# Optimization experiments

Measured on AMD Instinct MI355X. Metric: run time of the kernel, lower is better.

Reference implementation:

```python
import jax, jax.numpy as jnp
import numpy as np

NEG_SLOPE = 0.2  # PyG GATConv default leaky_relu slope


def gat_conv(x, src, dst, W, att_src, att_dst, bias, num_nodes):
    """PyG-style GATConv with concat=False (mean over heads).
    x: [N, Fin], src/dst: [E] (self-loops already appended),
    W: [Fin, H*C], att_src/att_dst: [H, C], bias: [C].
    """
    H, C = att_src.shape
    h = (x @ W).reshape(num_nodes, H, C)               # [N, H, C]
    a_s = jnp.sum(h * att_src[None], axis=-1)          # [N, H]
    a_d = jnp.sum(h * att_dst[None], axis=-1)          # [N, H]
    e = jax.nn.leaky_relu(a_s[src] + a_d[dst], NEG_SLOPE)  # [E, H]
    # softmax over incoming edges per destination node
    e_max = jax.ops.segment_max(e, dst, num_segments=num_nodes)  # [N, H]
    e_exp = jnp.exp(e - e_max[dst])
    denom = jax.ops.segment_sum(e_exp, dst, num_segments=num_nodes)
    alpha = e_exp / (denom[dst] + 1e-16)               # [E, H]
    msg = h[src] * alpha[:, :, None]                   # [E, H, C]
    out = jax.ops.segment_sum(msg, dst, num_segments=num_nodes)  # [N, H, C]
    return out.mean(axis=1) + bias                     # concat=False -> head mean


def setup_inputs() -> dict:
    N, E = 100000, 1600000
    Fin, Hid, Fout, Hds = 128, 64, 32, 2
    key = jax.random.key(0)
    ks = jax.random.split(key, 12)
    glorot = lambda k, shape, fan: (jax.random.normal(k, shape, jnp.float32) / np.sqrt(fan))
    return {
        "x": jax.random.normal(ks[0], (N, Fin), jnp.float32),
        "edge_index": jax.random.randint(ks[1], (2, E), 0, N, jnp.int64 if jax.config.read("jax_enable_x64") else jnp.int32),
        "W1": glorot(ks[2], (Fin, Hds * Hid), Fin),
        "att_src1": glorot(ks[3], (Hds, Hid), Hid),
        "att_dst1": glorot(ks[4], (Hds, Hid), Hid),
        "b1": jnp.zeros((Hid,), jnp.float32),
        "W2": glorot(ks[5], (Hid, Hds * Fout), Hid),
        "att_src2": glorot(ks[6], (Hds, Fout), Fout),
        "att_dst2": glorot(ks[7], (Hds, Fout), Fout),
        "b2": jnp.zeros((Fout,), jnp.float32),
    }


def reference(x, edge_index, W1, att_src1, att_dst1, b1, W2, att_src2, att_dst2, b2):
    N = x.shape[0]
    # PyG GATConv default: add self-loops
    loops = jnp.arange(N, dtype=edge_index.dtype)
    src = jnp.concatenate([edge_index[0], loops])
    dst = jnp.concatenate([edge_index[1], loops])
    # dropout(p=0.6) is identity in eval mode
    h = gat_conv(x, src, dst, W1, att_src1, att_dst1, b1, N)
    h = jax.nn.elu(h)
    out = gat_conv(h, src, dst, W2, att_src2, att_dst2, b2, N)
    return out
```

## Files before the change

kernel.cpp:

```cpp
#include <hip/hip_runtime.h>
#include <hip/hip_bf16.h>
#include <hip/hip_fp16.h>
#include <math.h>


#define BINBITS 9
#define NBUCK 256
#define CHUNK 4096
#define SPANCAP 12288

typedef _Float16 half8 __attribute__((ext_vector_type(8)));
typedef float f32x4 __attribute__((ext_vector_type(4)));


__global__ void init_kernel(int* __restrict__ bcnt) {
    bcnt[threadIdx.x] = 0;
}

__global__ void bucket_hist_kernel(const int* __restrict__ dst, int* __restrict__ bcnt, int E) {
    __shared__ int h[NBUCK];
    int t = threadIdx.x;
    h[t] = 0;
    __syncthreads();
    for (int i = blockIdx.x * blockDim.x + t; i < E; i += gridDim.x * blockDim.x)
        atomicAdd(&h[dst[i] >> BINBITS], 1);
    __syncthreads();
    if (h[t]) atomicAdd(&bcnt[t], h[t]);
}

__global__ void bucket_scan_kernel(const int* __restrict__ bcnt, int* __restrict__ bbase,
                                   int* __restrict__ bfill) {
    __shared__ int sd[NBUCK];
    int t = threadIdx.x;
    int v = bcnt[t];
    sd[t] = v;
    __syncthreads();
    for (int o = 1; o < NBUCK; o <<= 1) {
        int x = (t >= o) ? sd[t - o] : 0;
        __syncthreads();
        sd[t] += x;
        __syncthreads();
    }
    int exc = sd[t] - v;
    bbase[t] = exc;
    bfill[t] = exc;
    if (t == NBUCK - 1) bbase[NBUCK] = sd[t];
}

__launch_bounds__(256)
__global__ void binA_kernel(const int* __restrict__ esrc, const int* __restrict__ edst,
                            int* __restrict__ bfill, unsigned* __restrict__ binned, int E) {
    __shared__ unsigned stage[CHUNK];
    __shared__ int hcnt[NBUCK], hexc[NBUCK], gb[NBUCK], hfill[NBUCK];
    const int tid = threadIdx.x;
    const int c0 = blockIdx.x * CHUNK;
    const int n = min(CHUNK, E - c0);

    hcnt[tid] = 0;
    hfill[tid] = 0;
    __syncthreads();
    for (int i = tid; i < n; i += 256) atomicAdd(&hcnt[edst[c0 + i] >> BINBITS], 1);
    __syncthreads();
    int myc = hcnt[tid];
    hexc[tid] = myc;
    __syncthreads();
    for (int o = 1; o < NBUCK; o <<= 1) {
        int x = (tid >= o) ? hexc[tid - o] : 0;
        __syncthreads();
        hexc[tid] += x;
        __syncthreads();
    }
    hexc[tid] -= myc;
    gb[tid] = myc ? atomicAdd(&bfill[tid], myc) : 0;
    __syncthreads();

    for (int i = tid; i < n; i += 256) {
        int d = edst[c0 + i], s = esrc[c0 + i];
        int b = d >> BINBITS;
        int p = hexc[b] + atomicAdd(&hfill[b], 1);
        stage[p] = ((unsigned)(d & ((1 << BINBITS) - 1)) << 17) | (unsigned)s;
    }
    __syncthreads();

    const int wid = tid >> 6, lane = tid & 63;
    for (int b = wid * 64; b < wid * 64 + 64; ++b) {
        int cnt = hcnt[b], sb = hexc[b], g = gb[b];
        for (int l = lane; l < cnt; l += 64) binned[g + l] = stage[sb + l];
    }
}

__launch_bounds__(256)
__global__ void binB_kernel(const unsigned* __restrict__ binned, const int* __restrict__ bbase,
                            int* __restrict__ rowptr, int* __restrict__ csr, int N) {
    __shared__ int cnt[512];
    __shared__ int chunk[256];
    __shared__ int excl[513];
    __shared__ int stag[SPANCAP];
    const int tid = threadIdx.x;
    const int b = blockIdx.x;
    const int node0 = b << BINBITS;
    if (node0 >= N) return;
    const int nn = min(512, N - node0);

    cnt[tid] = (tid < nn) ? 1 : 0;
    cnt[tid + 256] = (tid + 256 < nn) ? 1 : 0;
    __syncthreads();
    const int e0 = bbase[b], e1 = bbase[b + 1];
    for (int i = e0 + tid; i < e1; i += 256)
        atomicAdd(&cnt[binned[i] >> 17], 1);
    __syncthreads();

    int c0v = cnt[2 * tid], c1v = cnt[2 * tid + 1];
    chunk[tid] = c0v + c1v;
    __syncthreads();
    int v = chunk[tid];
    for (int o = 1; o < 256; o <<= 1) {
        int x = (tid >= o) ? chunk[tid - o] : 0;
        __syncthreads();
        chunk[tid] += x;
        __syncthreads();
    }
    int cpre = chunk[tid] - v;
    excl[2 * tid] = cpre;
    excl[2 * tid + 1] = cpre + c0v;
    if (tid == 255) excl[512] = cpre + c0v + c1v;
    __syncthreads();

    const int rbase = e0 + node0;
    for (int i = tid; i < nn; i += 256) rowptr[node0 + i] = rbase + excl[i];
    if (node0 + nn >= N && tid == 0) rowptr[N] = rbase + excl[512];

    cnt[tid] = 0;
    cnt[tid + 256] = 0;
    __syncthreads();
    const int span = excl[512];

    if (span <= SPANCAP) {
        for (int i = e0 + tid; i < e1; i += 256) {
            unsigned e = binned[i];
            int dloc = e >> 17, src = e & 0x1FFFF;
            int p = excl[dloc] + atomicAdd(&cnt[dloc], 1);
            stag[p] = src;
        }
        for (int i = tid; i < nn; i += 256) {
            int p = excl[i] + atomicAdd(&cnt[i], 1);
            stag[p] = node0 + i;
        }
        __syncthreads();
        for (int i = tid; i < span; i += 256) csr[rbase + i] = stag[i];
    } else {
        for (int i = e0 + tid; i < e1; i += 256) {
            unsigned e = binned[i];
            int dloc = e >> 17, src = e & 0x1FFFF;
            csr[rbase + excl[dloc] + atomicAdd(&cnt[dloc], 1)] = src;
        }
        for (int i = tid; i < nn; i += 256)
            csr[rbase + excl[i] + atomicAdd(&cnt[i], 1)] = node0 + i;
    }
}


__global__ void wcvt_kernel(const float* __restrict__ W, _Float16* __restrict__ Wt,
                            int K, int Fout) {
    int i = blockIdx.x * 256 + threadIdx.x;
    if (i < K * Fout) {
        int n = i / K, k = i % K;
        Wt[i] = (_Float16)W[k * Fout + n];
    }
}


template <int FIN, int FOUT, typename XT>
__launch_bounds__(256)
__global__ void gemm_attn_mfma(const XT* __restrict__ X, const _Float16* __restrict__ Wt,
                               const float* __restrict__ atts, const float* __restrict__ attd,
                               __half* __restrict__ Hh, float* __restrict__ a_s,
                               float* __restrict__ a_d, int N) {
    constexpr int BM = 128;
    constexpr int C = FOUT / 2;
    constexpr int NT = FOUT / 16;
    constexpr int KS = FIN / 32;
    constexpr int HT = C / 16;
    __shared__ _Float16 sA[BM * FIN];
    __shared__ _Float16 sB[FOUT * FIN];

    const int tid = threadIdx.x;
    const int wv = tid >> 6, ln = tid & 63;
    const int lm = ln & 15, quad = ln >> 4;
    const int row0 = blockIdx.x * BM;

    if (sizeof(XT) == 4) {
        for (int idx = tid; idx < BM * FIN / 4; idx += 256) {
            int r = idx / (FIN / 4), c4 = idx % (FIN / 4);
            int gr = row0 + r;
            float4 v = make_float4(0.f, 0.f, 0.f, 0.f);
            if (gr < N) v = *(const float4*)&((const float*)X)[(size_t)gr * FIN + c4 * 4];
            _Float16 h4[4] = {(_Float16)v.x, (_Float16)v.y, (_Float16)v.z, (_Float16)v.w};
            *(float2*)&sA[r * FIN + c4 * 4] = *(float2*)h4;
        }
    } else {
        for (int idx = tid; idx < BM * FIN / 8; idx += 256) {
            int r = idx / (FIN / 8), c8 = idx % (FIN / 8);
            int gr = row0 + r;
            int4 v = make_int4(0, 0, 0, 0);
            if (gr < N) v = *(const int4*)&((const __half*)X)[(size_t)gr * FIN + c8 * 8];
            *(int4*)&sA[r * FIN + c8 * 8] = v;
        }
    }
    for (int idx = tid; idx < FOUT * FIN / 8; idx += 256)
        *(int4*)&sB[idx * 8] = *(const int4*)&Wt[idx * 8];
    __syncthreads();

    f32x4 acc[2][NT];
#pragma unroll
    for (int mt = 0; mt < 2; ++mt)
#pragma unroll
        for (int nt = 0; nt < NT; ++nt) acc[mt][nt] = f32x4{0.f, 0.f, 0.f, 0.f};

    const int r0 = wv * 32 + lm;
#pragma unroll
    for (int ks = 0; ks < KS; ++ks) {
        int k0 = ks * 32 + quad * 8;
        half8 a0 = *(const half8*)&sA[r0 * FIN + k0];
        half8 a1 = *(const half8*)&sA[(r0 + 16) * FIN + k0];
#pragma unroll
        for (int nt = 0; nt < NT; ++nt) {
            half8 b = *(const half8*)&sB[(nt * 16 + lm) * FIN + k0];
            acc[0][nt] = __builtin_amdgcn_mfma_f32_16x16x32_f16(a0, b, acc[0][nt], 0, 0, 0);
            acc[1][nt] = __builtin_amdgcn_mfma_f32_16x16x32_f16(a1, b, acc[1][nt], 0, 0, 0);
        }
    }

    float psum[2][4][2], pdum[2][4][2];
#pragma unroll
    for (int mt = 0; mt < 2; ++mt)
#pragma unroll
        for (int r = 0; r < 4; ++r) {
            psum[mt][r][0] = psum[mt][r][1] = 0.f;
            pdum[mt][r][0] = pdum[mt][r][1] = 0.f;
        }
#pragma unroll
    for (int nt = 0; nt < NT; ++nt) {
        float av = atts[nt * 16 + lm];
        float dv = attd[nt * 16 + lm];
        int hh = nt / HT;
#pragma unroll
        for (int mt = 0; mt < 2; ++mt)
#pragma unroll
            for (int r = 0; r < 4; ++r) {
                psum[mt][r][hh] = fmaf(acc[mt][nt][r], av, psum[mt][r][hh]);
                pdum[mt][r][hh] = fmaf(acc[mt][nt][r], dv, pdum[mt][r][hh]);
            }
    }
#pragma unroll
    for (int o = 1; o < 16; o <<= 1) {
#pragma unroll
        for (int mt = 0; mt < 2; ++mt)
#pragma unroll
            for (int r = 0; r < 4; ++r) {
                psum[mt][r][0] += __shfl_xor(psum[mt][r][0], o);
                psum[mt][r][1] += __shfl_xor(psum[mt][r][1], o);
                pdum[mt][r][0] += __shfl_xor(pdum[mt][r][0], o);
                pdum[mt][r][1] += __shfl_xor(pdum[mt][r][1], o);
            }
    }
    if (lm == 0) {
#pragma unroll
        for (int mt = 0; mt < 2; ++mt)
#pragma unroll
            for (int r = 0; r < 4; ++r) {
                int gr = row0 + wv * 32 + mt * 16 + quad * 4 + r;
                if (gr < N) {
                    *(float2*)&a_s[gr * 2] = make_float2(psum[mt][r][0], psum[mt][r][1]);
                    *(float2*)&a_d[gr * 2] = make_float2(pdum[mt][r][0], pdum[mt][r][1]);
                }
            }
    }

    __syncthreads();
    _Float16* sH = sA;
#pragma unroll
    for (int mt = 0; mt < 2; ++mt)
#pragma unroll
        for (int nt = 0; nt < NT; ++nt)
#pragma unroll
            for (int r = 0; r < 4; ++r)
                sH[(wv * 32 + mt * 16 + quad * 4 + r) * FOUT + nt * 16 + lm] =
                    (_Float16)acc[mt][nt][r];
    __syncthreads();
    for (int idx = tid; idx < BM * FOUT / 8; idx += 256) {
        int r = idx / (FOUT / 8), c8 = idx % (FOUT / 8);
        int gr = row0 + r;
        if (gr < N)
            *(int4*)&Hh[(size_t)gr * FOUT + c8 * 8] = *(const int4*)&sH[r * FOUT + c8 * 8];
    }
}


__device__ __forceinline__ float lrelu02(float x) { return x > 0.f ? x : 0.2f * x; }

__launch_bounds__(256)
__global__ void edge_w_kernel(const float* __restrict__ a_s, const float* __restrict__ a_d,
                              const int* __restrict__ rowptr, const int* __restrict__ csr,
                              float2* __restrict__ w, int N) {
    const int wid = threadIdx.x >> 6, lane = threadIdx.x & 63;
    int n = blockIdx.x * 4 + wid;
    if (n >= N) return;
    int start = rowptr[n], end = rowptr[n + 1];
    float2 adn = ((const float2*)a_d)[n];
    float d0 = 0.f, d1 = 0.f;
    for (int j = start + lane; j < end; j += 64) {
        int s = csr[j];
        float2 asv = ((const float2*)a_s)[s];
        float e0 = __expf(lrelu02(asv.x + adn.x));
        float e1 = __expf(lrelu02(asv.y + adn.y));
        d0 += e0;
        d1 += e1;
        w[j] = make_float2(e0, e1);
    }
#pragma unroll
    for (int o = 32; o > 0; o >>= 1) {
        d0 += __shfl_xor(d0, o);
        d1 += __shfl_xor(d1, o);
    }
    float i0 = 0.5f / d0, i1 = 0.5f / d1;
    for (int j = start + lane; j < end; j += 64) {
        float2 f = w[j];
        w[j] = make_float2(f.x * i0, f.y * i1);
    }
}


template <int C, bool ELU, typename OT>
__launch_bounds__(256)
__global__ void aggregate_kernel(const __half* __restrict__ Hh, const float2* __restrict__ w,
                                 const int* __restrict__ rowptr, const int* __restrict__ csr,
                                 const float* __restrict__ bias, OT* __restrict__ out, int N) {
    __shared__ float2 swH[4][64][2];
    const int wid = threadIdx.x >> 6;
    const int lane = threadIdx.x & 63;
    const int hp = lane >> 5;
    const int sub = lane & 31;
    const int head = sub >> 4;
    const int chq = sub & 15;
    int n = blockIdx.x * 4 + wid;
    if (n >= N) return;
    int start = rowptr[n], end = rowptr[n + 1];

    float acc0 = 0.f, acc1 = 0.f, acc2 = 0.f, acc3 = 0.f;

    for (int cs = start; cs < end; cs += 64) {
        int j = cs + lane;
        float2 wv = make_float2(0.f, 0.f);
        int s = 0;
        if (j < end) {
            s = csr[j];
            wv = w[j];
        }
        float fs = __int_as_float(s);
        swH[wid][lane][0] = make_float2(wv.x, fs);
        swH[wid][lane][1] = make_float2(wv.y, fs);
        int cnt = min(64, end - cs);
        int npair = (cnt + 1) >> 1;
        for (int p0 = 0; p0 < npair; p0 += 4) {
            float2 e[4];
#pragma unroll
            for (int u = 0; u < 4; ++u)
                e[u] = swH[wid][2 * (p0 + u) + hp][head];
            if (C == 64) {
                ushort4 hv[4];
#pragma unroll
                for (int u = 0; u < 4; ++u)
                    hv[u] = ((const ushort4*)Hh)[(size_t)__float_as_int(e[u].y) * 32 + sub];
#pragma unroll
                for (int u = 0; u < 4; ++u) {
                    const __half* hx = (const __half*)&hv[u];
                    acc0 = fmaf(e[u].x, __half2float(hx[0]), acc0);
                    acc1 = fmaf(e[u].x, __half2float(hx[1]), acc1);
                    acc2 = fmaf(e[u].x, __half2float(hx[2]), acc2);
                    acc3 = fmaf(e[u].x, __half2float(hx[3]), acc3);
                }
            } else {
                __half2 hv[4];
#pragma unroll
                for (int u = 0; u < 4; ++u)
                    hv[u] = ((const __half2*)Hh)[(size_t)__float_as_int(e[u].y) * 32 + sub];
#pragma unroll
                for (int u = 0; u < 4; ++u) {
                    float2 v = __half22float2(hv[u]);
                    acc0 = fmaf(e[u].x, v.x, acc0);
                    acc1 = fmaf(e[u].x, v.y, acc1);
                }
            }
        }
    }

    acc0 += __shfl_xor(acc0, 32);
    acc1 += __shfl_xor(acc1, 32);
    if (C == 64) {
        acc2 += __shfl_xor(acc2, 32);
        acc3 += __shfl_xor(acc3, 32);
    }
    acc0 += __shfl_xor(acc0, 16);
    acc1 += __shfl_xor(acc1, 16);
    if (C == 64) {
        acc2 += __shfl_xor(acc2, 16);
        acc3 += __shfl_xor(acc3, 16);
    }

    if (lane < 16) {
        if (C == 64) {
            float4 bv = *(const float4*)(bias + chq * 4);
            float o0 = acc0 + bv.x;
            float o1 = acc1 + bv.y;
            float o2 = acc2 + bv.z;
            float o3 = acc3 + bv.w;
            if (ELU) {
                o0 = o0 > 0.f ? o0 : expm1f(o0);
                o1 = o1 > 0.f ? o1 : expm1f(o1);
                o2 = o2 > 0.f ? o2 : expm1f(o2);
                o3 = o3 > 0.f ? o3 : expm1f(o3);
            }
            if (sizeof(OT) == 2) {
                __half2 p0 = __floats2half2_rn(o0, o1);
                __half2 p1 = __floats2half2_rn(o2, o3);
                ((__half2*)out)[(size_t)n * 32 + chq * 2] = p0;
                ((__half2*)out)[(size_t)n * 32 + chq * 2 + 1] = p1;
            } else {
                *(float4*)((float*)out + (size_t)n * 64 + chq * 4) =
                    make_float4(o0, o1, o2, o3);
            }
        } else {
            float2 bv = *(const float2*)(bias + chq * 2);
            float o0 = acc0 + bv.x;
            float o1 = acc1 + bv.y;
            if (ELU) {
                o0 = o0 > 0.f ? o0 : expm1f(o0);
                o1 = o1 > 0.f ? o1 : expm1f(o1);
            }
            *(float2*)((float*)out + (size_t)n * 32 + chq * 2) = make_float2(o0, o1);
        }
    }
}


extern "C" void kernel_launch(void* const* d_in, const int* in_sizes, int n_in,
                              void* d_out, int out_size, void* d_ws, size_t ws_size,
                              hipStream_t stream) {
    const float* x    = (const float*)d_in[0];
    const int*   eidx = (const int*)d_in[1];
    const float* W1   = (const float*)d_in[2];
    const float* as1w = (const float*)d_in[3];
    const float* ad1w = (const float*)d_in[4];
    const float* b1   = (const float*)d_in[5];
    const float* W2   = (const float*)d_in[6];
    const float* as2w = (const float*)d_in[7];
    const float* ad2w = (const float*)d_in[8];
    const float* b2   = (const float*)d_in[9];
    float* out = (float*)d_out;

    const int N = in_sizes[0] / 128;
    const int E = in_sizes[1] / 2;
    const int NBK = (N + (1 << BINBITS) - 1) >> BINBITS;

    char* base = (char*)d_ws;
    size_t off = 0;
    auto alloc = [&](size_t bytes) {
        size_t cur = off;
        off += (bytes + 255) & ~(size_t)255;
        return (void*)(base + cur);
    };

    int* rowptr   = (int*)alloc((size_t)(N + 1) * 4);
    int* csr      = (int*)alloc((size_t)(E + N) * 4);
    int* bcnt     = (int*)alloc((size_t)NBUCK * 4);
    int* bbase    = (int*)alloc((size_t)(NBUCK + 1) * 4);
    int* bfill    = (int*)alloc((size_t)NBUCK * 4);
    unsigned* binned = (unsigned*)alloc((size_t)E * 4);
    __half* h1    = (__half*)alloc((size_t)N * 128 * 2);
    __half* x2h   = (__half*)alloc((size_t)N * 64 * 2);
    float* a_s    = (float*)alloc((size_t)N * 2 * 4);
    float* a_d    = (float*)alloc((size_t)N * 2 * 4);
    float2* wEdge = (float2*)alloc((size_t)(E + N) * 8);
    _Float16* Wt1 = (_Float16*)alloc((size_t)128 * 128 * 2);
    _Float16* Wt2 = (_Float16*)alloc((size_t)64 * 64 * 2);

    const int* esrc = eidx;
    const int* edst = eidx + E;

    init_kernel<<<1, NBUCK, 0, stream>>>(bcnt);
    bucket_hist_kernel<<<256, 256, 0, stream>>>(edst, bcnt, E);
    bucket_scan_kernel<<<1, NBUCK, 0, stream>>>(bcnt, bbase, bfill);
    binA_kernel<<<(E + CHUNK - 1) / CHUNK, 256, 0, stream>>>(esrc, edst, bfill, binned, E);
    binB_kernel<<<NBK, 256, 0, stream>>>(binned, bbase, rowptr, csr, N);

    wcvt_kernel<<<(128 * 128 + 255) / 256, 256, 0, stream>>>(W1, Wt1, 128, 128);
    wcvt_kernel<<<(64 * 64 + 255) / 256, 256, 0, stream>>>(W2, Wt2, 64, 64);

    gemm_attn_mfma<128, 128, float>
        <<<(N + 127) / 128, 256, 0, stream>>>(x, Wt1, as1w, ad1w, h1, a_s, a_d, N);
    edge_w_kernel<<<(N + 3) / 4, 256, 0, stream>>>(a_s, a_d, rowptr, csr, wEdge, N);
    aggregate_kernel<64, true, __half>
        <<<(N + 3) / 4, 256, 0, stream>>>(h1, wEdge, rowptr, csr, b1, x2h, N);

    gemm_attn_mfma<64, 64, __half>
        <<<(N + 127) / 128, 256, 0, stream>>>(x2h, Wt2, as2w, ad2w, h1, a_s, a_d, N);
    edge_w_kernel<<<(N + 3) / 4, 256, 0, stream>>>(a_s, a_d, rowptr, csr, wEdge, N);
    aggregate_kernel<32, false, float>
        <<<(N + 3) / 4, 256, 0, stream>>>(h1, wEdge, rowptr, csr, b2, out, N);
}
```

Baseline: 374.6 us.

## Widen aggregate gathers to 16-byte loads, add single-pass edge softmax, merge weight conversions

```diff
diff --git a/kernel.cpp b/kernel.cpp
--- a/kernel.cpp
+++ b/kernel.cpp
@@ -160,12 +160,17 @@
 }
 
 
-__global__ void wcvt_kernel(const float* __restrict__ W, _Float16* __restrict__ Wt,
-                            int K, int Fout) {
+__global__ void wcvt_kernel(const float* __restrict__ W1, _Float16* __restrict__ Wt1,
+                            const float* __restrict__ W2, _Float16* __restrict__ Wt2) {
     int i = blockIdx.x * 256 + threadIdx.x;
-    if (i < K * Fout) {
-        int n = i / K, k = i % K;
-        Wt[i] = (_Float16)W[k * Fout + n];
+    if (i < 128 * 128) {
+        int n = i >> 7, k = i & 127;
+        Wt1[i] = (_Float16)W1[k * 128 + n];
+    }
+    int j = i - 128 * 128;
+    if (j >= 0 && j < 64 * 64) {
+        int n = j >> 6, k = j & 63;
+        Wt2[j] = (_Float16)W2[k * 64 + n];
     }
 }
 
@@ -307,26 +312,47 @@
     int n = blockIdx.x * 4 + wid;
     if (n >= N) return;
     int start = rowptr[n], end = rowptr[n + 1];
+    int deg = end - start;
     float2 adn = ((const float2*)a_d)[n];
-    float d0 = 0.f, d1 = 0.f;
-    for (int j = start + lane; j < end; j += 64) {
-        int s = csr[j];
-        float2 asv = ((const float2*)a_s)[s];
-        float e0 = __expf(lrelu02(asv.x + adn.x));
-        float e1 = __expf(lrelu02(asv.y + adn.y));
-        d0 += e0;
-        d1 += e1;
-        w[j] = make_float2(e0, e1);
-    }
-#pragma unroll
-    for (int o = 32; o > 0; o >>= 1) {
-        d0 += __shfl_xor(d0, o);
-        d1 += __shfl_xor(d1, o);
-    }
-    float i0 = 0.5f / d0, i1 = 0.5f / d1;
-    for (int j = start + lane; j < end; j += 64) {
-        float2 f = w[j];
-        w[j] = make_float2(f.x * i0, f.y * i1);
+
+    if (deg <= 64) {
+        float e0 = 0.f, e1 = 0.f;
+        int j = start + lane;
+        if (lane < deg) {
+            int s = csr[j];
+            float2 asv = ((const float2*)a_s)[s];
+            e0 = __expf(lrelu02(asv.x + adn.x));
+            e1 = __expf(lrelu02(asv.y + adn.y));
+        }
+        float d0 = e0, d1 = e1;
+#pragma unroll
+        for (int o = 32; o > 0; o >>= 1) {
+            d0 += __shfl_xor(d0, o);
+            d1 += __shfl_xor(d1, o);
+        }
+        float i0 = 0.5f / d0, i1 = 0.5f / d1;
+        if (lane < deg) w[j] = make_float2(e0 * i0, e1 * i1);
+    } else {
+        float d0 = 0.f, d1 = 0.f;
+        for (int j = start + lane; j < end; j += 64) {
+            int s = csr[j];
+            float2 asv = ((const float2*)a_s)[s];
+            float e0 = __expf(lrelu02(asv.x + adn.x));
+            float e1 = __expf(lrelu02(asv.y + adn.y));
+            d0 += e0;
+            d1 += e1;
+            w[j] = make_float2(e0, e1);
+        }
+#pragma unroll
+        for (int o = 32; o > 0; o >>= 1) {
+            d0 += __shfl_xor(d0, o);
+            d1 += __shfl_xor(d1, o);
+        }
+        float i0 = 0.5f / d0, i1 = 0.5f / d1;
+        for (int j = start + lane; j < end; j += 64) {
+            float2 f = w[j];
+            w[j] = make_float2(f.x * i0, f.y * i1);
+        }
     }
 }
 
@@ -336,18 +362,23 @@
 __global__ void aggregate_kernel(const __half* __restrict__ Hh, const float2* __restrict__ w,
                                  const int* __restrict__ rowptr, const int* __restrict__ csr,
                                  const float* __restrict__ bias, OT* __restrict__ out, int N) {
-    __shared__ float2 swH[4][64][2];
+    constexpr int LPE = (C == 64) ? 16 : 8;
+    constexpr int NG = 64 / LPE;
+    constexpr int RI = C / 4;
+    __shared__ float4 swR[4][64];
     const int wid = threadIdx.x >> 6;
     const int lane = threadIdx.x & 63;
-    const int hp = lane >> 5;
-    const int sub = lane & 31;
-    const int head = sub >> 4;
-    const int chq = sub & 15;
+    const int sub = lane & (LPE - 1);
+    const int qid = lane / LPE;
+    const int isH1 = (sub >= LPE / 2);
     int n = blockIdx.x * 4 + wid;
     if (n >= N) return;
     int start = rowptr[n], end = rowptr[n + 1];
-
-    float acc0 = 0.f, acc1 = 0.f, acc2 = 0.f, acc3 = 0.f;
+    const int4* HI = (const int4*)Hh;
+
+    float av[8];
+#pragma unroll
+    for (int j = 0; j < 8; ++j) av[j] = 0.f;
 
     for (int cs = start; cs < end; cs += 64) {
         int j = cs + lane;
@@ -357,88 +388,61 @@
             s = csr[j];
             wv = w[j];
         }
-        float fs = __int_as_float(s);
-        swH[wid][lane][0] = make_float2(wv.x, fs);
-        swH[wid][lane][1] = make_float2(wv.y, fs);
+        swR[wid][lane] = make_float4(wv.x, wv.y, __int_as_float(s), 0.f);
         int cnt = min(64, end - cs);
-        int npair = (cnt + 1) >> 1;
-        for (int p0 = 0; p0 < npair; p0 += 4) {
-            float2 e[4];
+        int nbatch = (cnt + NG - 1) / NG;
+        for (int b = 0; b < nbatch; b += 4) {
+            float4 r[4];
 #pragma unroll
             for (int u = 0; u < 4; ++u)
-                e[u] = swH[wid][2 * (p0 + u) + hp][head];
-            if (C == 64) {
-                ushort4 hv[4];
-#pragma unroll
-                for (int u = 0; u < 4; ++u)
-                    hv[u] = ((const ushort4*)Hh)[(size_t)__float_as_int(e[u].y) * 32 + sub];
-#pragma unroll
-                for (int u = 0; u < 4; ++u) {
-                    const __half* hx = (const __half*)&hv[u];
-                    acc0 = fmaf(e[u].x, __half2float(hx[0]), acc0);
-                    acc1 = fmaf(e[u].x, __half2float(hx[1]), acc1);
-                    acc2 = fmaf(e[u].x, __half2float(hx[2]), acc2);
-                    acc3 = fmaf(e[u].x, __half2float(hx[3]), acc3);
-                }
-            } else {
-                __half2 hv[4];
-#pragma unroll
-                for (int u = 0; u < 4; ++u)
-                    hv[u] = ((const __half2*)Hh)[(size_t)__float_as_int(e[u].y) * 32 + sub];
-#pragma unroll
-                for (int u = 0; u < 4; ++u) {
-                    float2 v = __half22float2(hv[u]);
-                    acc0 = fmaf(e[u].x, v.x, acc0);
-                    acc1 = fmaf(e[u].x, v.y, acc1);
+                r[u] = swR[wid][(b + u) * NG + qid];
+            int4 hv[4];
+#pragma unroll
+            for (int u = 0; u < 4; ++u)
+                hv[u] = HI[(size_t)__float_as_int(r[u].z) * RI + sub];
+#pragma unroll
+            for (int u = 0; u < 4; ++u) {
+                float ww = isH1 ? r[u].y : r[u].x;
+                const __half2* h2 = (const __half2*)&hv[u];
+#pragma unroll
+                for (int p = 0; p < 4; ++p) {
+                    float2 f = __half22float2(h2[p]);
+                    av[2 * p] = fmaf(ww, f.x, av[2 * p]);
+                    av[2 * p + 1] = fmaf(ww, f.y, av[2 * p + 1]);
                 }
             }
         }
     }
 
-    acc0 += __shfl_xor(acc0, 32);
-    acc1 += __shfl_xor(acc1, 32);
-    if (C == 64) {
-        acc2 += __shfl_xor(acc2, 32);
-        acc3 += __shfl_xor(acc3, 32);
-    }
-    acc0 += __shfl_xor(acc0, 16);
-    acc1 += __shfl_xor(acc1, 16);
-    if (C == 64) {
-        acc2 += __shfl_xor(acc2, 16);
-        acc3 += __shfl_xor(acc3, 16);
-    }
-
-    if (lane < 16) {
-        if (C == 64) {
-            float4 bv = *(const float4*)(bias + chq * 4);
-            float o0 = acc0 + bv.x;
-            float o1 = acc1 + bv.y;
-            float o2 = acc2 + bv.z;
-            float o3 = acc3 + bv.w;
-            if (ELU) {
-                o0 = o0 > 0.f ? o0 : expm1f(o0);
-                o1 = o1 > 0.f ? o1 : expm1f(o1);
-                o2 = o2 > 0.f ? o2 : expm1f(o2);
-                o3 = o3 > 0.f ? o3 : expm1f(o3);
-            }
-            if (sizeof(OT) == 2) {
-                __half2 p0 = __floats2half2_rn(o0, o1);
-                __half2 p1 = __floats2half2_rn(o2, o3);
-                ((__half2*)out)[(size_t)n * 32 + chq * 2] = p0;
-                ((__half2*)out)[(size_t)n * 32 + chq * 2 + 1] = p1;
-            } else {
-                *(float4*)((float*)out + (size_t)n * 64 + chq * 4) =
-                    make_float4(o0, o1, o2, o3);
-            }
+#pragma unroll
+    for (int o = LPE; o < 64; o <<= 1)
+#pragma unroll
+        for (int j = 0; j < 8; ++j) av[j] += __shfl_xor(av[j], o);
+#pragma unroll
+    for (int j = 0; j < 8; ++j) av[j] += __shfl_xor(av[j], LPE / 2);
+
+    if (lane < LPE / 2) {
+        float4 b0 = *(const float4*)(bias + sub * 8);
+        float4 b1 = *(const float4*)(bias + sub * 8 + 4);
+        float o0[8];
+        o0[0] = av[0] + b0.x; o0[1] = av[1] + b0.y;
+        o0[2] = av[2] + b0.z; o0[3] = av[3] + b0.w;
+        o0[4] = av[4] + b1.x; o0[5] = av[5] + b1.y;
+        o0[6] = av[6] + b1.z; o0[7] = av[7] + b1.w;
+        if (ELU) {
+#pragma unroll
+            for (int j = 0; j < 8; ++j) o0[j] = o0[j] > 0.f ? o0[j] : expm1f(o0[j]);
+        }
+        if (sizeof(OT) == 2) {
+            union { int4 v; __half2 h2[4]; } u;
+#pragma unroll
+            for (int p = 0; p < 4; ++p) u.h2[p] = __floats2half2_rn(o0[2 * p], o0[2 * p + 1]);
+            *(int4*)((__half*)out + (size_t)n * C + sub * 8) = u.v;
         } else {
-            float2 bv = *(const float2*)(bias + chq * 2);
-            float o0 = acc0 + bv.x;
-            float o1 = acc1 + bv.y;
-            if (ELU) {
-                o0 = o0 > 0.f ? o0 : expm1f(o0);
-                o1 = o1 > 0.f ? o1 : expm1f(o1);
-            }
-            *(float2*)((float*)out + (size_t)n * 32 + chq * 2) = make_float2(o0, o1);
+            *(float4*)((float*)out + (size_t)n * C + sub * 8) =
+                make_float4(o0[0], o0[1], o0[2], o0[3]);
+            *(float4*)((float*)out + (size_t)n * C + sub * 8 + 4) =
+                make_float4(o0[4], o0[5], o0[6], o0[7]);
         }
     }
 }
@@ -494,8 +498,7 @@
     binA_kernel<<<(E + CHUNK - 1) / CHUNK, 256, 0, stream>>>(esrc, edst, bfill, binned, E);
     binB_kernel<<<NBK, 256, 0, stream>>>(binned, bbase, rowptr, csr, N);
 
-    wcvt_kernel<<<(128 * 128 + 255) / 256, 256, 0, stream>>>(W1, Wt1, 128, 128);
-    wcvt_kernel<<<(64 * 64 + 255) / 256, 256, 0, stream>>>(W2, Wt2, 64, 64);
+    wcvt_kernel<<<(128 * 128 + 64 * 64 + 255) / 256, 256, 0, stream>>>(W1, Wt1, W2, Wt2);
 
     gemm_attn_mfma<128, 128, float>
         <<<(N + 127) / 128, 256, 0, stream>>>(x, Wt1, as1w, ad1w, h1, a_s, a_d, N);
```

Measured after the change: 520.5 us. 39.0% more time.
